# Kernel tuning notes

Measured on AMD Instinct MI355X. Metric: run time of the kernel, lower is better.

Reference implementation:

```python
import jax, jax.numpy as jnp
import numpy as np

B, N, C = 4, 1024, 1024
H = 16
D = C // H
FF = 4 * C
EPS = 1e-5


def setup_inputs() -> dict:
    key = jax.random.key(0)
    ks = jax.random.split(key, 16)
    s = 0.02
    return {
        "x": jax.random.normal(ks[0], (B, N, C), jnp.float32),
        "c": jax.random.normal(ks[1], (B, C), jnp.float32),
        "node_mask": jax.random.randint(ks[2], (B, N), 0, 2) > 0,
        "qkv_w": jax.random.normal(ks[3], (C, 3 * C), jnp.float32) * s,
        "proj_w": jax.random.normal(ks[4], (C, C), jnp.float32) * s,
        "proj_b": jnp.zeros((C,), jnp.float32),
        "fc1_w": jax.random.normal(ks[5], (C, FF), jnp.float32) * s,
        "fc1_b": jnp.zeros((FF,), jnp.float32),
        "fc2_w": jax.random.normal(ks[6], (FF, C), jnp.float32) * s,
        "fc2_b": jnp.zeros((C,), jnp.float32),
        "ada1_w": jax.random.normal(ks[7], (C, C), jnp.float32) * s,
        "ada1_b": jnp.zeros((C,), jnp.float32),
        "ada2_w": jax.random.normal(ks[8], (C, 6 * C), jnp.float32) * s,
        "ada2_b": jnp.zeros((6 * C,), jnp.float32),
    }


def _layernorm(x):
    # LayerNorm without affine params (elementwise_affine=False), eps=1e-5
    mu = jnp.mean(x, axis=-1, keepdims=True)
    var = jnp.mean(jnp.square(x - mu), axis=-1, keepdims=True)
    return (x - mu) * jax.lax.rsqrt(var + EPS)


def _modulate(x, shift, scale):
    return x * (1.0 + scale[:, None, :]) + shift[:, None, :]


def _attention(x, node_mask, qkv_w, proj_w, proj_b):
    b, n, c = x.shape
    qkv = (x @ qkv_w).reshape(b, n, 3, H, D)
    q, k, v = jnp.moveaxis(qkv, 2, 0)          # each [b, n, H, D]
    q = q.transpose(0, 2, 1, 3)                # [b, H, n, D]
    k = k.transpose(0, 2, 1, 3)
    v = v.transpose(0, 2, 1, 3)
    scale = D ** -0.5
    scores = jnp.einsum("bhnd,bhmd->bhnm", q, k) * scale
    mask = node_mask[:, None, None, :]          # key mask [b,1,1,n]
    scores = jnp.where(mask, scores, -jnp.inf)
    attn = jax.nn.softmax(scores, axis=-1)
    out = jnp.einsum("bhnm,bhmd->bhnd", attn, v)
    out = out.transpose(0, 2, 1, 3).reshape(b, n, c)
    return out @ proj_w + proj_b


def _mlp(x, fc1_w, fc1_b, fc2_w, fc2_b):
    h = jax.nn.gelu(x @ fc1_w + fc1_b, approximate=False)
    return h @ fc2_w + fc2_b


def reference(x, c, node_mask, qkv_w, proj_w, proj_b, fc1_w, fc1_b,
              fc2_w, fc2_b, ada1_w, ada1_b, ada2_w, ada2_b):
    # adaLN: Linear -> SiLU -> Linear -> 6 chunks along feature dim
    ada = jax.nn.silu(c @ ada1_w + ada1_b) @ ada2_w + ada2_b
    (shift_msa, scale_msa, gate_msa,
     shift_mlp, scale_mlp, gate_mlp) = jnp.split(ada, 6, axis=1)

    attn_out = _attention(x, node_mask, qkv_w, proj_w, proj_b)
    x = x + gate_msa[:, None, :] * _modulate(_layernorm(attn_out), shift_msa, scale_msa)

    mlp_out = _mlp(x, fc1_w, fc1_b, fc2_w, fc2_b)
    x = x + gate_mlp[:, None, :] * _modulate(_layernorm(mlp_out), shift_mlp, scale_mlp)
    return x
```

## Files before the change

### kernel.cpp

```cpp
#include <hip/hip_runtime.h>

typedef unsigned short u16;
typedef __attribute__((ext_vector_type(8))) short short8;
typedef __attribute__((ext_vector_type(8))) unsigned short u16x8;
typedef __attribute__((ext_vector_type(4))) unsigned short u16x4;
typedef __attribute__((ext_vector_type(4))) float f32x4;

#define DEVINL __device__ __forceinline__

DEVINL u16 f2b(float f) {
    union { float f; unsigned u; } a; a.f = f;
    unsigned r = a.u + 0x7FFFu + ((a.u >> 16) & 1u);
    return (u16)(r >> 16);
}
DEVINL float b2f(u16 h) {
    union { unsigned u; float f; } a; a.u = ((unsigned)h) << 16;
    return a.f;
}

DEVINL void gload16(const void* g, void* l) {
    __builtin_amdgcn_global_load_lds(
        (const __attribute__((address_space(1))) void*)g,
        (__attribute__((address_space(3))) void*)l, 16, 0, 0);
}

__global__ void detect_mask(const unsigned char* __restrict__ m, int nbytes, int* __restrict__ flag) {
    __shared__ int any;
    if (threadIdx.x == 0) any = 0;
    __syncthreads();
    int loc = 0;
    for (int i = threadIdx.x; i < nbytes; i += 256)
        if ((i & 3) && m[i]) loc = 1;
    if (loc) atomicOr(&any, 1);
    __syncthreads();
    if (threadIdx.x == 0) *flag = any;
}

__global__ __launch_bounds__(256) void f32_to_bf16(const float* __restrict__ in, u16* __restrict__ out, int n4) {
    int i = blockIdx.x * 256 + threadIdx.x;
    if (i >= n4) return;
    float4 v = ((const float4*)in)[i];
    u16x4 o = { f2b(v.x), f2b(v.y), f2b(v.z), f2b(v.w) };
    *(u16x4*)(out + (size_t)i * 4) = o;
}

__global__ __launch_bounds__(256) void transpose_bf16(const float* __restrict__ W, u16* __restrict__ WT, int K, int N) {
    __shared__ float tile[32][33];
    int tx = threadIdx.x, ty = threadIdx.y;
    int n0 = blockIdx.x * 32, k0 = blockIdx.y * 32;
#pragma unroll
    for (int i = 0; i < 4; i++)
        tile[ty + i * 8][tx] = W[(size_t)(k0 + ty + i * 8) * N + n0 + tx];
    __syncthreads();
#pragma unroll
    for (int i = 0; i < 4; i++)
        WT[(size_t)(n0 + ty + i * 8) * K + k0 + tx] = f2b(tile[tx][ty + i * 8]);
}

__global__ __launch_bounds__(256) void transpose_v(const u16* __restrict__ qkv, u16* __restrict__ vtg) {
    __shared__ u16 tile[64][72];
    const int bh = blockIdx.x & 63, nt = blockIdx.x >> 6;
    const int b = bh >> 4, h = bh & 15;
    const int t = threadIdx.x;
    const int r = t >> 3, c = (t & 7) << 3;
#pragma unroll
    for (int i = 0; i < 2; i++) {
        int rr = r + i * 32;
        *(u16x8*)&tile[rr][c] =
            *(const u16x8*)&qkv[(size_t)(b * 1024 + nt * 64 + rr) * 3072 + 2048 + h * 64 + c];
    }
    __syncthreads();
#pragma unroll
    for (int i = 0; i < 2; i++) {
        int d = r + i * 32;
        u16x8 o;
#pragma unroll
        for (int e = 0; e < 8; e++) o[e] = tile[c + e][d];
        *(u16x8*)&vtg[(size_t)bh * 65536 + (size_t)d * 1024 + nt * 64 + c] = o;
    }
}

template <int KRLOG2>
__global__ __launch_bounds__(256) void gemv_partial(
    const float* __restrict__ h, const float* __restrict__ w,
    float* __restrict__ part, int N, int K) {
    constexpr int KR = 1 << KRLOG2;
    constexpr int KR4 = KR >> 2;
    __shared__ float hs[4 * KR];
    __shared__ float red[256 * 16];
    const int t = threadIdx.x, wv = t >> 6, l = t & 63;
    const int j4 = blockIdx.x * 256 + l * 4;
    const int kb = blockIdx.y << KRLOG2;
    for (int idx = t; idx < 4 * KR; idx += 256) {
        int b = idx >> KRLOG2, kk = idx & (KR - 1);
        hs[idx] = h[b * K + kb + kk];
    }
    __syncthreads();
    float acc[4][4];
#pragma unroll
    for (int b = 0; b < 4; b++)
#pragma unroll
        for (int c = 0; c < 4; c++) acc[b][c] = 0.f;
    const float* wp = w + (size_t)(kb + wv * KR4) * N + j4;
#pragma unroll
    for (int i = 0; i < KR4; i++) {
        float4 wf = *(const float4*)(wp + (size_t)i * N);
        int kk = wv * KR4 + i;
#pragma unroll
        for (int b = 0; b < 4; b++) {
            float hv = hs[(b << KRLOG2) + kk];
            acc[b][0] += hv * wf.x;
            acc[b][1] += hv * wf.y;
            acc[b][2] += hv * wf.z;
            acc[b][3] += hv * wf.w;
        }
    }
#pragma unroll
    for (int b = 0; b < 4; b++)
#pragma unroll
        for (int c = 0; c < 4; c++)
            red[t * 16 + b * 4 + c] = acc[b][c];
    __syncthreads();
    if (t < 64) {
#pragma unroll
        for (int b = 0; b < 4; b++) {
            float4 s;
            s.x = red[l * 16 + b * 4 + 0] + red[(l + 64) * 16 + b * 4 + 0] + red[(l + 128) * 16 + b * 4 + 0] + red[(l + 192) * 16 + b * 4 + 0];
            s.y = red[l * 16 + b * 4 + 1] + red[(l + 64) * 16 + b * 4 + 1] + red[(l + 128) * 16 + b * 4 + 1] + red[(l + 192) * 16 + b * 4 + 1];
            s.z = red[l * 16 + b * 4 + 2] + red[(l + 64) * 16 + b * 4 + 2] + red[(l + 128) * 16 + b * 4 + 2] + red[(l + 192) * 16 + b * 4 + 2];
            s.w = red[l * 16 + b * 4 + 3] + red[(l + 64) * 16 + b * 4 + 3] + red[(l + 128) * 16 + b * 4 + 3] + red[(l + 192) * 16 + b * 4 + 3];
            *(float4*)&part[(size_t)(blockIdx.y * 4 + b) * N + j4] = s;
        }
    }
}

template <int SILU>
__global__ __launch_bounds__(256) void gemv_reduce(
    const float* __restrict__ part, const float* __restrict__ bias,
    float* __restrict__ out, int N, int NK) {
    int gid = blockIdx.x * 256 + threadIdx.x;
    int b = gid / N, j = gid - b * N;
    float s = bias[j];
    for (int i = 0; i < NK; i++) s += part[(size_t)(i * 4 + b) * N + j];
    if (SILU) s = s / (1.f + __expf(-s));
    out[gid] = s;
}

template <int EPI>
__global__ __launch_bounds__(256) void gemm_bt64(
    const u16* __restrict__ A, const u16* __restrict__ B, const float* __restrict__ bias,
    float* __restrict__ Cf, u16* __restrict__ Cb, int M, int N, int lda, int Ksub) {
    __shared__ u16 As[2][128 * 64];
    __shared__ u16 Bs[2][128 * 64];
    const int t = threadIdx.x;
    const int w = t >> 6, l = t & 63;
    const int l15 = l & 15, lg = l >> 4;
    const int nTN = N >> 7;
    const int ntiles = (M >> 7) * nTN;
    const int sk = blockIdx.x / ntiles;
    int tb = blockIdx.x - sk * ntiles;
    tb = (tb & 7) * (ntiles >> 3) + (tb >> 3);
    const int tm = tb / nTN, tn = tb - tm * nTN;
    const int row0 = tm << 7, col0 = tn << 7;
    const int wr = (w >> 1) << 6, wc = (w & 1) << 6;
    const int k_begin = sk * Ksub;

    const int rA = t >> 3;
    const int cswz = ((t & 7) ^ (rA & 7)) << 3;
    const u16* gA = A + (size_t)(row0 + rA) * lda + cswz + k_begin;
    const u16* gB = B + (size_t)(col0 + rA) * lda + cswz + k_begin;
    const int rsw = l15 & 7;

    f32x4 acc[4][4];
#pragma unroll
    for (int i = 0; i < 4; i++)
#pragma unroll
        for (int j = 0; j < 4; j++) acc[i][j] = (f32x4){0.f, 0.f, 0.f, 0.f};

    const int nsteps = Ksub >> 6;
#pragma unroll
    for (int j = 0; j < 4; j++) {
        gload16(gA + (size_t)j * 32 * lda, As[0] + j * 2048 + w * 512);
        gload16(gB + (size_t)j * 32 * lda, Bs[0] + j * 2048 + w * 512);
    }
    __syncthreads();

    for (int it = 0; it < nsteps; ++it) {
        const int cur = it & 1;
        if (it + 1 < nsteps) {
            const int k0 = (it + 1) << 6;
#pragma unroll
            for (int j = 0; j < 4; j++) {
                gload16(gA + (size_t)j * 32 * lda + k0, As[cur ^ 1] + j * 2048 + w * 512);
                gload16(gB + (size_t)j * 32 * lda + k0, Bs[cur ^ 1] + j * 2048 + w * 512);
            }
        }
        __builtin_amdgcn_s_setprio(1);
#pragma unroll
        for (int ks = 0; ks < 2; ks++) {
            short8 af[4], bfr[4];
            const int chunk = ((ks << 2) + lg) ^ rsw;
#pragma unroll
            for (int mi = 0; mi < 4; mi++)
                af[mi] = *(const short8*)&As[cur][((wr + mi * 16 + l15) << 6) + (chunk << 3)];
#pragma unroll
            for (int ni = 0; ni < 4; ni++)
                bfr[ni] = *(const short8*)&Bs[cur][((wc + ni * 16 + l15) << 6) + (chunk << 3)];
#pragma unroll
            for (int mi = 0; mi < 4; mi++)
#pragma unroll
                for (int ni = 0; ni < 4; ni++)
                    acc[mi][ni] = __builtin_amdgcn_mfma_f32_16x16x32_bf16(af[mi], bfr[ni], acc[mi][ni], 0, 0, 0);
        }
        __builtin_amdgcn_s_setprio(0);
        __syncthreads();
    }

    float* Cfp = Cf ? Cf + (size_t)sk * M * N : nullptr;
    u16* Cbp = Cb ? Cb + (size_t)sk * M * N : nullptr;
#pragma unroll
    for (int mi = 0; mi < 4; mi++) {
#pragma unroll
        for (int ni = 0; ni < 4; ni++) {
#pragma unroll
            for (int j = 0; j < 4; j++) {
                int r = row0 + wr + mi * 16 + (lg << 2) + j;
                int c = col0 + wc + ni * 16 + l15;
                float v = acc[mi][ni][j];
                if (EPI == 0) {
                    Cbp[(size_t)r * N + c] = f2b(v);
                } else if (EPI == 2) {
                    float vv = v + bias[c];
                    float g = 0.5f * vv * (1.f + erff(vv * 0.70710678118f));
                    Cbp[(size_t)r * N + c] = f2b(g);
                } else {
                    Cfp[(size_t)r * N + c] = v;
                }
            }
        }
    }
}

__global__ __launch_bounds__(256) void attn_kernel(
    const u16* __restrict__ qkv, const u16* __restrict__ vtg,
    const unsigned char* __restrict__ maskb,
    const int* __restrict__ flagp, u16* __restrict__ out) {
    __shared__ u16 Qs[64 * 64];
    __shared__ u16 Ks[64 * 64];
    __shared__ u16 Vt[64 * 64];
    __shared__ u16 Ps[64 * 64];
    __shared__ float maskf[64];
    __shared__ float alpha_lds[64];
    __shared__ float lst_lds[64];

    int bi = (int)blockIdx.x;
    bi = (bi & 7) * 128 + (bi >> 3);
    const int qt = bi & 15, h = (bi >> 4) & 15, b = bi >> 8;
    const int t = threadIdx.x, w = t >> 6, l = t & 63;
    const int l15 = l & 15, lg = l >> 4;
    const int rsw = l15 & 7;
    const int flag = *flagp;
    const int q0 = qt << 6;
    const int bh = b * 16 + h;

    const int sr = t >> 3, sc = t & 7;
#pragma unroll
    for (int i = 0; i < 2; i++) {
        int r = sr + i * 32;
        u16x8 v = *(const u16x8*)&qkv[(size_t)(b * 1024 + q0 + r) * 3072 + h * 64 + sc * 8];
        u16x8 o;
#pragma unroll
        for (int e = 0; e < 8; e++) o[e] = f2b(b2f(v[e]) * 0.125f);
        *(u16x8*)&Qs[r * 64 + ((sc ^ (r & 7)) << 3)] = o;
    }

    f32x4 O[4];
#pragma unroll
    for (int nd = 0; nd < 4; nd++) O[nd] = (f32x4){0.f, 0.f, 0.f, 0.f};
    float mst = -1e30f, lst = 0.f;

    u16x8 kreg[2], vreg[2];
    float mnext;
    {
#pragma unroll
        for (int i = 0; i < 2; i++) {
            kreg[i] = *(const u16x8*)&qkv[(size_t)(b * 1024 + sr + i * 32) * 3072 + h * 64 + 1024 + sc * 8];
            vreg[i] = *(const u16x8*)&vtg[(size_t)bh * 65536 + (size_t)(sr + i * 32) * 1024 + sc * 8];
        }
        int gi = b * 1024 + (t & 63);
        bool ms = flag ? (maskb[gi] != 0) : (((const int*)maskb)[gi] != 0);
        mnext = ms ? 1.f : 0.f;
    }

    for (int kt = 0; kt < 16; kt++) {
        __syncthreads();
#pragma unroll
        for (int i = 0; i < 2; i++) {
            int r = sr + i * 32;
            *(u16x8*)&Ks[r * 64 + ((sc ^ (r & 7)) << 3)] = kreg[i];
            *(u16x8*)&Vt[r * 64 + ((sc ^ (r & 7)) << 3)] = vreg[i];
        }
        if (t < 64) maskf[t] = mnext;
        __syncthreads();
        if (kt < 15) {
            const int kn = (kt + 1) << 6;
#pragma unroll
            for (int i = 0; i < 2; i++) {
                kreg[i] = *(const u16x8*)&qkv[(size_t)(b * 1024 + kn + sr + i * 32) * 3072 + h * 64 + 1024 + sc * 8];
                vreg[i] = *(const u16x8*)&vtg[(size_t)bh * 65536 + (size_t)(sr + i * 32) * 1024 + kn + sc * 8];
            }
            int gi = b * 1024 + kn + (t & 63);
            bool ms = flag ? (maskb[gi] != 0) : (((const int*)maskb)[gi] != 0);
            mnext = ms ? 1.f : 0.f;
        }

        f32x4 S[4];
#pragma unroll
        for (int mi = 0; mi < 4; mi++) S[mi] = (f32x4){0.f, 0.f, 0.f, 0.f};
        __builtin_amdgcn_s_setprio(1);
#pragma unroll
        for (int ks = 0; ks < 2; ks++) {
            const int chunk = (((ks << 2) + lg) ^ rsw) << 3;
            short8 bq = *(const short8*)&Qs[(w * 16 + l15) * 64 + chunk];
#pragma unroll
            for (int mi = 0; mi < 4; mi++) {
                short8 ak = *(const short8*)&Ks[(mi * 16 + l15) * 64 + chunk];
                S[mi] = __builtin_amdgcn_mfma_f32_16x16x32_bf16(ak, bq, S[mi], 0, 0, 0);
            }
        }
        __builtin_amdgcn_s_setprio(0);

        float pm = -1e30f;
#pragma unroll
        for (int mi = 0; mi < 4; mi++) {
            f32x4 mk = *(const f32x4*)&maskf[mi * 16 + (lg << 2)];
#pragma unroll
            for (int j = 0; j < 4; j++) {
                float xv = (mk[j] > 0.f) ? S[mi][j] : -1e30f;
                S[mi][j] = xv;
                pm = fmaxf(pm, xv);
            }
        }
        pm = fmaxf(pm, __shfl_xor(pm, 16));
        pm = fmaxf(pm, __shfl_xor(pm, 32));

        bool skip = __all(pm <= mst + 8.f);
        float alpha = 1.f;
        if (!skip) {
            float mn = fmaxf(mst, pm);
            alpha = __expf(mst - mn);
            mst = mn;
        }

        float psum = 0.f;
        const int prow = w * 16 + l15;
#pragma unroll
        for (int mi = 0; mi < 4; mi++) {
            f32x4 mk = *(const f32x4*)&maskf[mi * 16 + (lg << 2)];
            u16x4 v4;
#pragma unroll
            for (int j = 0; j < 4; j++) {
                float p = __expf(S[mi][j] - mst) * mk[j];
                psum += p;
                v4[j] = f2b(p);
            }
            int ch = ((mi * 2 + (lg >> 1)) ^ rsw);
            *(u16x4*)&Ps[prow * 64 + (ch << 3) + ((lg & 1) << 2)] = v4;
        }
        psum += __shfl_xor(psum, 16);
        psum += __shfl_xor(psum, 32);
        lst = lst * alpha + psum;

        if (!skip) {
            if (lg == 0) alpha_lds[w * 16 + l15] = alpha;
            f32x4 af = *(const f32x4*)&alpha_lds[w * 16 + (lg << 2)];
#pragma unroll
            for (int nd = 0; nd < 4; nd++)
#pragma unroll
                for (int j = 0; j < 4; j++) O[nd][j] *= af[j];
        }

        __builtin_amdgcn_s_setprio(1);
#pragma unroll
        for (int ks = 0; ks < 2; ks++) {
            const int chunk = (((ks << 2) + lg) ^ rsw) << 3;
            short8 pa = *(const short8*)&Ps[(w * 16 + l15) * 64 + chunk];
#pragma unroll
            for (int nd = 0; nd < 4; nd++) {
                short8 bv = *(const short8*)&Vt[(nd * 16 + l15) * 64 + chunk];
                O[nd] = __builtin_amdgcn_mfma_f32_16x16x32_bf16(pa, bv, O[nd], 0, 0, 0);
            }
        }
        __builtin_amdgcn_s_setprio(0);
    }

    if (lg == 0) lst_lds[w * 16 + l15] = lst;
    f32x4 lf = *(const f32x4*)&lst_lds[w * 16 + (lg << 2)];
#pragma unroll
    for (int nd = 0; nd < 4; nd++)
#pragma unroll
        for (int j = 0; j < 4; j++) {
            int r = b * 1024 + q0 + w * 16 + (lg << 2) + j;
            int c = h * 64 + nd * 16 + l15;
            out[(size_t)r * 1024 + c] = f2b(O[nd][j] / lf[j]);
        }
}

template <int BF>
__global__ __launch_bounds__(256) void ln_mod_res2(
    const void* __restrict__ s0, const void* __restrict__ s1, const float* __restrict__ bias,
    const float* __restrict__ resid, const float* __restrict__ ada, int oS, int oC, int oG,
    float* __restrict__ outf, u16* __restrict__ outb) {
    __shared__ float red[8];
    const int row = blockIdx.x, t = threadIdx.x, b = row >> 10;
    const float4 bv = ((const float4*)bias)[t];
    float4 v;
    if (BF) {
        u16x4 a0 = *(const u16x4*)((const u16*)s0 + (size_t)row * 1024 + t * 4);
        u16x4 a1 = *(const u16x4*)((const u16*)s1 + (size_t)row * 1024 + t * 4);
        v.x = b2f(a0[0]) + b2f(a1[0]) + bv.x;
        v.y = b2f(a0[1]) + b2f(a1[1]) + bv.y;
        v.z = b2f(a0[2]) + b2f(a1[2]) + bv.z;
        v.w = b2f(a0[3]) + b2f(a1[3]) + bv.w;
    } else {
        float4 a0 = ((const float4*)((const float*)s0 + (size_t)row * 1024))[t];
        float4 a1 = ((const float4*)((const float*)s1 + (size_t)row * 1024))[t];
        v.x = a0.x + a1.x + bv.x;
        v.y = a0.y + a1.y + bv.y;
        v.z = a0.z + a1.z + bv.z;
        v.w = a0.w + a1.w + bv.w;
    }
    float s = v.x + v.y + v.z + v.w;
    float q = v.x * v.x + v.y * v.y + v.z * v.z + v.w * v.w;
#pragma unroll
    for (int off = 32; off >= 1; off >>= 1) {
        s += __shfl_down(s, off);
        q += __shfl_down(q, off);
    }
    if ((t & 63) == 0) { red[(t >> 6) * 2] = s; red[(t >> 6) * 2 + 1] = q; }
    __syncthreads();
    float sum = red[0] + red[2] + red[4] + red[6];
    float sq = red[1] + red[3] + red[5] + red[7];
    float mu = sum * (1.f / 1024.f);
    float var = sq * (1.f / 1024.f) - mu * mu;
    float rinv = rsqrtf(var + 1e-5f);
    const float* ad = ada + b * 6144;
    const float4 rv = ((const float4*)(resid + (size_t)row * 1024))[t];
    const float4 sc = ((const float4*)(ad + oC))[t];
    const float4 sh = ((const float4*)(ad + oS))[t];
    const float4 gt = ((const float4*)(ad + oG))[t];
    float4 o;
    o.x = rv.x + gt.x * ((v.x - mu) * rinv * (1.f + sc.x) + sh.x);
    o.y = rv.y + gt.y * ((v.y - mu) * rinv * (1.f + sc.y) + sh.y);
    o.z = rv.z + gt.z * ((v.z - mu) * rinv * (1.f + sc.z) + sh.z);
    o.w = rv.w + gt.w * ((v.w - mu) * rinv * (1.f + sc.w) + sh.w);
    ((float4*)(outf + (size_t)row * 1024))[t] = o;
    if (outb) {
        u16x4 ob = { f2b(o.x), f2b(o.y), f2b(o.z), f2b(o.w) };
        *(u16x4*)(outb + (size_t)row * 1024 + t * 4) = ob;
    }
}

extern "C" void kernel_launch(void* const* d_in, const int* in_sizes, int n_in,
                              void* d_out, int out_size, void* d_ws, size_t ws_size,
                              hipStream_t stream) {
    (void)in_sizes; (void)n_in; (void)out_size; (void)ws_size;
    const float* x = (const float*)d_in[0];
    const float* cvec = (const float*)d_in[1];
    const unsigned char* maskb = (const unsigned char*)d_in[2];
    const float* qkv_w = (const float*)d_in[3];
    const float* proj_w = (const float*)d_in[4];
    const float* proj_b = (const float*)d_in[5];
    const float* fc1_w = (const float*)d_in[6];
    const float* fc1_b = (const float*)d_in[7];
    const float* fc2_w = (const float*)d_in[8];
    const float* fc2_b = (const float*)d_in[9];
    const float* ada1_w = (const float*)d_in[10];
    const float* ada1_b = (const float*)d_in[11];
    const float* ada2_w = (const float*)d_in[12];
    const float* ada2_b = (const float*)d_in[13];
    float* outp = (float*)d_out;

    char* ws = (char*)d_ws;
    size_t off = 0;
    auto nxt = [&](size_t bytes) { size_t r = off; off += (bytes + 255) & ~(size_t)255; return r; };
    u16* qkvwT  = (u16*)(ws + nxt(3072ull * 1024 * 2));
    u16* projwT = (u16*)(ws + nxt(1024ull * 1024 * 2));
    u16* fc1wT  = (u16*)(ws + nxt(4096ull * 1024 * 2));
    u16* fc2wT  = (u16*)(ws + nxt(1024ull * 4096 * 2));
    float* adah = (float*)(ws + nxt(4ull * 1024 * 4));
    float* ada  = (float*)(ws + nxt(4ull * 6144 * 4));
    float* part1 = (float*)(ws + nxt(32ull * 4 * 1024 * 4));
    float* part2 = (float*)(ws + nxt(8ull * 4 * 6144 * 4));
    int* flag   = (int*)(ws + nxt(256));
    u16* xbf = (u16*)(ws + nxt(4096ull * 1024 * 2));
    u16* attn_buf = xbf;
    char* regC = ws + nxt(2ull * 4096 * 1024 * 4);
    u16* qkvbf = (u16*)regC;
    float* projpart = (float*)regC;
    u16* hbuf = (u16*)regC;
    float* y1 = (float*)(ws + nxt(4096ull * 1024 * 4));
    u16* y1b = (u16*)(ws + nxt(4096ull * 1024 * 2));
    u16* fc2part = (u16*)(ws + nxt(2ull * 4096 * 1024 * 2));
    u16* vtg = fc2part;

    detect_mask<<<1, 256, 0, stream>>>(maskb, 4096, flag);
    f32_to_bf16<<<4096, 256, 0, stream>>>(x, xbf, 1048576);
    transpose_bf16<<<dim3(96, 32), dim3(32, 8), 0, stream>>>(qkv_w, qkvwT, 1024, 3072);
    transpose_bf16<<<dim3(32, 32), dim3(32, 8), 0, stream>>>(proj_w, projwT, 1024, 1024);
    transpose_bf16<<<dim3(128, 32), dim3(32, 8), 0, stream>>>(fc1_w, fc1wT, 1024, 4096);
    transpose_bf16<<<dim3(32, 128), dim3(32, 8), 0, stream>>>(fc2_w, fc2wT, 4096, 1024);

    gemv_partial<5><<<dim3(4, 32), 256, 0, stream>>>(cvec, ada1_w, part1, 1024, 1024);
    gemv_reduce<1><<<16, 256, 0, stream>>>(part1, ada1_b, adah, 1024, 32);
    gemv_partial<7><<<dim3(24, 8), 256, 0, stream>>>(adah, ada2_w, part2, 6144, 1024);
    gemv_reduce<0><<<96, 256, 0, stream>>>(part2, ada2_b, ada, 6144, 8);

    gemm_bt64<0><<<768, 256, 0, stream>>>(xbf, qkvwT, nullptr, nullptr, qkvbf, 4096, 3072, 1024, 1024);
    transpose_v<<<1024, 256, 0, stream>>>(qkvbf, vtg);
    attn_kernel<<<1024, 256, 0, stream>>>(qkvbf, vtg, maskb, flag, attn_buf);
    gemm_bt64<3><<<512, 256, 0, stream>>>(attn_buf, projwT, nullptr, projpart, nullptr, 4096, 1024, 1024, 512);
    ln_mod_res2<0><<<4096, 256, 0, stream>>>(projpart, projpart + 4096ull * 1024, proj_b,
                                             x, ada, 0, 1024, 2048, y1, y1b);
    gemm_bt64<2><<<1024, 256, 0, stream>>>(y1b, fc1wT, fc1_b, nullptr, hbuf, 4096, 4096, 1024, 1024);
    gemm_bt64<0><<<512, 256, 0, stream>>>(hbuf, fc2wT, nullptr, nullptr, fc2part, 4096, 1024, 4096, 2048);
    ln_mod_res2<1><<<4096, 256, 0, stream>>>(fc2part, fc2part + 4096ull * 1024, fc2_b,
                                             y1, ada, 3072, 4096, 5120, outp, nullptr);
}
```

Measured before the change: 281.1 us.

## Deepen GEMM LDS pipeline to prefetch two k-steps ahead with fine waitcnts

```diff
diff --git a/kernel.cpp b/kernel.cpp
--- a/kernel.cpp
+++ b/kernel.cpp
@@ -7,6 +7,7 @@
 typedef __attribute__((ext_vector_type(4))) float f32x4;
 
 #define DEVINL __device__ __forceinline__
+#define SGB0 __builtin_amdgcn_sched_barrier(0)
 
 DEVINL u16 f2b(float f) {
     union { float f; unsigned u; } a; a.f = f;
@@ -150,8 +151,8 @@
 __global__ __launch_bounds__(256) void gemm_bt64(
     const u16* __restrict__ A, const u16* __restrict__ B, const float* __restrict__ bias,
     float* __restrict__ Cf, u16* __restrict__ Cb, int M, int N, int lda, int Ksub) {
-    __shared__ u16 As[2][128 * 64];
-    __shared__ u16 Bs[2][128 * 64];
+    __shared__ u16 As[2][8192];
+    __shared__ u16 Bs[2][8192];
     const int t = threadIdx.x;
     const int w = t >> 6, l = t & 63;
     const int l15 = l & 15, lg = l >> 4;
@@ -178,42 +179,63 @@
         for (int j = 0; j < 4; j++) acc[i][j] = (f32x4){0.f, 0.f, 0.f, 0.f};
 
     const int nsteps = Ksub >> 6;
+
 #pragma unroll
     for (int j = 0; j < 4; j++) {
         gload16(gA + (size_t)j * 32 * lda, As[0] + j * 2048 + w * 512);
         gload16(gB + (size_t)j * 32 * lda, Bs[0] + j * 2048 + w * 512);
     }
-    __syncthreads();
+#pragma unroll
+    for (int j = 0; j < 4; j++) {
+        gload16(gA + (size_t)j * 32 * lda + 64, As[1] + j * 2048 + w * 512);
+        gload16(gB + (size_t)j * 32 * lda + 64, Bs[1] + j * 2048 + w * 512);
+    }
+    asm volatile("s_waitcnt vmcnt(8)" ::: "memory");
+    SGB0;
+    __builtin_amdgcn_s_barrier();
+    SGB0;
 
     for (int it = 0; it < nsteps; ++it) {
         const int cur = it & 1;
+        short8 af[2][4], bfr[2][4];
+#pragma unroll
+        for (int ks = 0; ks < 2; ks++) {
+            const int chunk = ((ks << 2) + lg) ^ rsw;
+#pragma unroll
+            for (int mi = 0; mi < 4; mi++)
+                af[ks][mi] = *(const short8*)&As[cur][((wr + mi * 16 + l15) << 6) + (chunk << 3)];
+#pragma unroll
+            for (int ni = 0; ni < 4; ni++)
+                bfr[ks][ni] = *(const short8*)&Bs[cur][((wc + ni * 16 + l15) << 6) + (chunk << 3)];
+        }
+        asm volatile("s_waitcnt lgkmcnt(0)" ::: "memory");
+        SGB0;
+        __builtin_amdgcn_s_barrier();
+        SGB0;
+        if (it + 2 < nsteps) {
+            const int k0 = (it + 2) << 6;
+#pragma unroll
+            for (int j = 0; j < 4; j++) {
+                gload16(gA + (size_t)j * 32 * lda + k0, As[cur] + j * 2048 + w * 512);
+                gload16(gB + (size_t)j * 32 * lda + k0, Bs[cur] + j * 2048 + w * 512);
+            }
+        }
+        __builtin_amdgcn_s_setprio(1);
+#pragma unroll
+        for (int ks = 0; ks < 2; ks++)
+#pragma unroll
+            for (int mi = 0; mi < 4; mi++)
+#pragma unroll
+                for (int ni = 0; ni < 4; ni++)
+                    acc[mi][ni] = __builtin_amdgcn_mfma_f32_16x16x32_bf16(af[ks][mi], bfr[ks][ni], acc[mi][ni], 0, 0, 0);
+        __builtin_amdgcn_s_setprio(0);
         if (it + 1 < nsteps) {
-            const int k0 = (it + 1) << 6;
-#pragma unroll
-            for (int j = 0; j < 4; j++) {
-                gload16(gA + (size_t)j * 32 * lda + k0, As[cur ^ 1] + j * 2048 + w * 512);
-                gload16(gB + (size_t)j * 32 * lda + k0, Bs[cur ^ 1] + j * 2048 + w * 512);
-            }
-        }
-        __builtin_amdgcn_s_setprio(1);
-#pragma unroll
-        for (int ks = 0; ks < 2; ks++) {
-            short8 af[4], bfr[4];
-            const int chunk = ((ks << 2) + lg) ^ rsw;
-#pragma unroll
-            for (int mi = 0; mi < 4; mi++)
-                af[mi] = *(const short8*)&As[cur][((wr + mi * 16 + l15) << 6) + (chunk << 3)];
-#pragma unroll
-            for (int ni = 0; ni < 4; ni++)
-                bfr[ni] = *(const short8*)&Bs[cur][((wc + ni * 16 + l15) << 6) + (chunk << 3)];
-#pragma unroll
-            for (int mi = 0; mi < 4; mi++)
-#pragma unroll
-                for (int ni = 0; ni < 4; ni++)
-                    acc[mi][ni] = __builtin_amdgcn_mfma_f32_16x16x32_bf16(af[mi], bfr[ni], acc[mi][ni], 0, 0, 0);
-        }
-        __builtin_amdgcn_s_setprio(0);
-        __syncthreads();
+            if (it + 2 < nsteps) asm volatile("s_waitcnt vmcnt(8)" ::: "memory");
+            else                 asm volatile("s_waitcnt vmcnt(0)" ::: "memory");
+            SGB0;
+            __builtin_amdgcn_s_barrier();
+            SGB0;
+        }
     }
 
     float* Cfp = Cf ? Cf + (size_t)sk * M * N : nullptr;
```

Result: faster. 274.4 us (-2.4%).
